# Kernel tuning notes

Hardware: AMD Instinct MI355X
Metric: run time of the kernel (lower is better)

Reference implementation:

```python
import jax, jax.numpy as jnp
import numpy as np

D = 768
H = 12
HD = D // H
NEG = -10000.0
EPS = 1e-12


def setup_inputs() -> dict:
    key = jax.random.key(0)
    ks = jax.random.split(key, 8)
    B, S = 4, 1024
    xavier = lambda k: jax.random.normal(k, (D, D), dtype=jnp.float32) * np.sqrt(2.0 / (D + D))
    return {
        "embeddings": jax.random.normal(ks[0], (B, S, D), dtype=jnp.float32),
        "padding_mask": jnp.ones((B, S), dtype=jnp.float32),
        "wq_w": xavier(ks[1]), "wq_b": jnp.zeros((D,), jnp.float32),
        "wk_w": xavier(ks[2]), "wk_b": jnp.zeros((D,), jnp.float32),
        "wv_w": xavier(ks[3]), "wv_b": jnp.zeros((D,), jnp.float32),
        "wo_w": xavier(ks[4]), "wo_b": jnp.zeros((D,), jnp.float32),
        "ln_g": jnp.ones((D,), jnp.float32), "ln_b": jnp.zeros((D,), jnp.float32),
    }


def reference(embeddings, padding_mask, wq_w, wq_b, wk_w, wk_b, wv_w, wv_b, wo_w, wo_b, ln_g, ln_b):
    B, S, _ = embeddings.shape
    # QKV projections (torch Linear: x @ W^T + b), split heads -> [B,H,S,HD]
    split = lambda t: t.reshape(B, S, H, HD).transpose(0, 2, 1, 3)
    q = split(embeddings @ wq_w.T + wq_b)
    k = split(embeddings @ wk_w.T + wk_b)
    v = split(embeddings @ wv_w.T + wv_b)
    # NOTE: original scales by sqrt(embedding_dim), not sqrt(per-head dim)
    attn = jnp.einsum("bhqd,bhkd->bhqk", q, k) / jnp.sqrt(jnp.float32(D))
    # additive padding mask, then causal masked_fill (set, not add)
    attn = attn + ((1.0 - padding_mask)[:, None, None, :] * NEG)
    causal = jnp.tril(jnp.ones((S, S), dtype=jnp.float32))
    attn = jnp.where(causal[None, None] == 0, NEG, attn)
    attn_probs = jax.nn.softmax(attn, axis=-1)  # dropout is identity at inference
    ctx = jnp.einsum("bhqk,bhkd->bhqd", attn_probs, v)
    ctx = ctx.transpose(0, 2, 1, 3).reshape(B, S, D)
    attn_out = ctx @ wo_w.T + wo_b  # keep_prob = 1.0 -> no rescale
    # residual + LayerNorm(eps=1e-12)
    x = attn_out + embeddings
    mu = jnp.mean(x, axis=-1, keepdims=True)
    var = jnp.mean((x - mu) ** 2, axis=-1, keepdims=True)
    normed = (x - mu) * jax.lax.rsqrt(var + EPS) * ln_g + ln_b
    return (normed, attn_probs)
```

## Files before the change

kernel.cpp:

```cpp
#include <hip/hip_runtime.h>
#include <hip/hip_bf16.h>

typedef __bf16 bf16x8 __attribute__((ext_vector_type(8)));
typedef float  f32x4  __attribute__((ext_vector_type(4)));

#define NEGC (-10000.0f)

static __device__ __forceinline__ void glds16(const __bf16* src, __bf16* dst) {
    __builtin_amdgcn_global_load_lds((const __attribute__((address_space(1))) unsigned int*)src,
                                     (__attribute__((address_space(3))) unsigned int*)dst, 16, 0, 0);
}

__global__ __launch_bounds__(256) void cvt_all(
    const float* __restrict__ emb, const float* __restrict__ wq, const float* __restrict__ wk,
    const float* __restrict__ wv, const float* __restrict__ wo,
    __bf16* __restrict__ Xb, __bf16* __restrict__ Wall)
{
    int blk = blockIdx.x;
    const float* src; __bf16* dst; int i;
    if (blk < 1536) {
        src = emb; dst = Xb; i = blk * 256 + threadIdx.x;
    } else {
        int b2 = blk - 1536;
        int which = b2 / 288;
        src = which == 0 ? wq : which == 1 ? wk : which == 2 ? wv : wo;
        dst = Wall + (size_t)which * 589824;
        i = (b2 - which * 288) * 256 + threadIdx.x;
    }
    f32x4 a = *(const f32x4*)(src + (size_t)i * 8);
    f32x4 b = *(const f32x4*)(src + (size_t)i * 8 + 4);
    bf16x8 o;
    o[0] = (__bf16)a[0]; o[1] = (__bf16)a[1]; o[2] = (__bf16)a[2]; o[3] = (__bf16)a[3];
    o[4] = (__bf16)b[0]; o[5] = (__bf16)b[1]; o[6] = (__bf16)b[2]; o[7] = (__bf16)b[3];
    *(bf16x8*)(dst + (size_t)i * 8) = o;
}

template<int MODE>
__global__ __launch_bounds__(256) void gemm128(
    const __bf16* __restrict__ A, const __bf16* __restrict__ Bw,
    const float* __restrict__ b0, const float* __restrict__ b1, const float* __restrict__ b2,
    __bf16* __restrict__ O0, __bf16* __restrict__ O1, __bf16* __restrict__ O2,
    const float* __restrict__ res, float* __restrict__ Yout)
{
    __shared__ __align__(16) __bf16 As[128 * 32];
    __shared__ __align__(16) __bf16 Bs[128 * 32];
    const int K = 768;
    int tid = threadIdx.x;
    int l = tid & 63, w = tid >> 6;
    int lo = l & 15, hi = l >> 4;
    int m0 = blockIdx.x * 128, n0 = blockIdx.y * 128;
    int wr = w >> 1, wc = w & 1;

    f32x4 acc[4][4] = {};

    int srow = w * 16 + (l >> 2);
    int scol = (l & 3) * 8;
    const __bf16* gA = A + (size_t)(m0 + srow) * K + scol;
    const __bf16* gB = Bw + (size_t)(n0 + srow) * K + scol;
    __bf16* lA = As + w * 512 + l * 8;
    __bf16* lB = Bs + w * 512 + l * 8;

    for (int k0 = 0; k0 < K; k0 += 32) {
        if (k0) __syncthreads();
        glds16(gA + k0, lA);
        glds16(gA + (size_t)64 * K + k0, lA + 2048);
        glds16(gB + k0, lB);
        glds16(gB + (size_t)64 * K + k0, lB + 2048);
        __syncthreads();

        bf16x8 af[4], bfr[4];
#pragma unroll
        for (int mi = 0; mi < 4; mi++)
            af[mi] = *(const bf16x8*)(As + (wr * 64 + mi * 16 + lo) * 32 + hi * 8);
#pragma unroll
        for (int ni = 0; ni < 4; ni++)
            bfr[ni] = *(const bf16x8*)(Bs + (wc * 64 + ni * 16 + lo) * 32 + hi * 8);
#pragma unroll
        for (int mi = 0; mi < 4; mi++)
#pragma unroll
            for (int ni = 0; ni < 4; ni++)
                acc[mi][ni] = __builtin_amdgcn_mfma_f32_16x16x32_bf16(af[mi], bfr[ni], acc[mi][ni], 0, 0, 0);
    }

    if constexpr (MODE == 0) {
        int which = n0 / 768;
        const float* bias = which == 0 ? b0 : (which == 1 ? b1 : b2);
        __bf16* O = which == 0 ? O0 : (which == 1 ? O1 : O2);
        int nbase = n0 - which * 768;
#pragma unroll
        for (int mi = 0; mi < 4; mi++)
#pragma unroll
            for (int ni = 0; ni < 4; ni++) {
                int within = nbase + wc * 64 + ni * 16 + lo;
                float bv = bias[within];
                int h = within >> 6, d = within & 63;
#pragma unroll
                for (int i = 0; i < 4; i++) {
                    int m = m0 + wr * 64 + mi * 16 + hi * 4 + i;
                    int bb = m >> 10, s = m & 1023;
                    O[(size_t)((bb * 12 + h) * 1024 + s) * 64 + d] = (__bf16)(acc[mi][ni][i] + bv);
                }
            }
    } else {
#pragma unroll
        for (int mi = 0; mi < 4; mi++)
#pragma unroll
            for (int ni = 0; ni < 4; ni++) {
                int n = n0 + wc * 64 + ni * 16 + lo;
                float bv = b0[n];
#pragma unroll
                for (int i = 0; i < 4; i++) {
                    int m = m0 + wr * 64 + mi * 16 + hi * 4 + i;
                    size_t idx = (size_t)m * 768 + n;
                    Yout[idx] = acc[mi][ni][i] + bv + res[idx];
                }
            }
    }
}

__global__ __launch_bounds__(256) void attn_kernel(
    const __bf16* __restrict__ Q, const __bf16* __restrict__ K, const __bf16* __restrict__ V,
    const float* __restrict__ pmask, float* __restrict__ Pout, __bf16* __restrict__ ctx)
{
    int wgid = blockIdx.x;
    int xcd = wgid & 7;
    int t = wgid >> 3;
    int bh = xcd * 6 + (t % 6);
    int y = t / 6;
    int b = bh / 12, h = bh - b * 12;
    int q0 = y * 64;
    int tid = threadIdx.x, l = tid & 63, w = tid >> 6;
    int lo = l & 15, hi = l >> 4;
    int qw = q0 + w * 16;

    const __bf16* Qh = Q + (size_t)bh * 65536;
    const __bf16* Kh = K + (size_t)bh * 65536;
    const __bf16* Vh = V + (size_t)bh * 65536;
    float* Ph = Pout + (size_t)bh * 1048576;
    const float* pm = pmask + b * 1024;

    __shared__ __align__(16) __bf16 Ks[2][64][64];
    __shared__ __align__(16) __bf16 vt[2][64][72];
    __shared__ __align__(16) __bf16 plds[4][16][72];

    const float scale = 0.036084391824351615f;

    bf16x8 qf0 = *(const bf16x8*)(Qh + (size_t)(qw + lo) * 64 + hi * 8);
    bf16x8 qf1 = *(const bf16x8*)(Qh + (size_t)(qw + lo) * 64 + 32 + hi * 8);

    int srow = tid >> 3;
    int scb  = (tid & 7) ^ (srow & 7);
    __bf16* ldst0 = &Ks[0][0][0] + tid * 8;

#define STAGE_K(buf, kt)  do {                                             \
        glds16(Kh + (size_t)((kt) * 64 + srow) * 64 + scb * 8,             \
               ldst0 + (buf) * 4096);                                      \
        glds16(Kh + (size_t)((kt) * 64 + 32 + srow) * 64 + scb * 8,        \
               ldst0 + (buf) * 4096 + 2048);                               \
    } while (0)

#define KFRAG(buf, kn, dh) \
    (*(const bf16x8*)(&Ks[buf][(kn) * 16 + lo][(((dh) * 4 + hi) ^ (lo & 7)) * 8]))

    float lsum[4] = {};
    STAGE_K(0, 0);
    __syncthreads();
    for (int kt = 0; kt <= y; kt++) {
        int cur = kt & 1;
        if (kt < y) STAGE_K(cur ^ 1, kt + 1);
        int k0 = kt * 64;
        float pad[4];
#pragma unroll
        for (int kn = 0; kn < 4; kn++) pad[kn] = (1.0f - pm[k0 + kn * 16 + lo]) * NEGC;
        f32x4 s[4] = {};
        __builtin_amdgcn_s_setprio(1);
#pragma unroll
        for (int kn = 0; kn < 4; kn++) {
            s[kn] = __builtin_amdgcn_mfma_f32_16x16x32_bf16(qf0, KFRAG(cur, kn, 0), s[kn], 0, 0, 0);
            s[kn] = __builtin_amdgcn_mfma_f32_16x16x32_bf16(qf1, KFRAG(cur, kn, 1), s[kn], 0, 0, 0);
        }
        __builtin_amdgcn_s_setprio(0);
#pragma unroll
        for (int kn = 0; kn < 4; kn++) {
            int c = k0 + kn * 16 + lo;
#pragma unroll
            for (int i = 0; i < 4; i++) {
                int r = qw + hi * 4 + i;
                float a = s[kn][i] * scale + pad[kn];
                if (c > r) a = NEGC;
                lsum[i] += __expf(a);
            }
        }
        __syncthreads();
    }

    float invl[4];
#pragma unroll
    for (int i = 0; i < 4; i++) {
        float s = lsum[i];
        s += __shfl_xor(s, 1);
        s += __shfl_xor(s, 2);
        s += __shfl_xor(s, 4);
        s += __shfl_xor(s, 8);
        invl[i] = 1.0f / s;
    }

    int vrow = tid >> 2, vcol = (tid & 3) * 16;
    bf16x8 va, vb;
    {
        STAGE_K(0, 0);
        const __bf16* vp = Vh + (size_t)vrow * 64 + vcol;
        va = *(const bf16x8*)vp; vb = *(const bf16x8*)(vp + 8);
#pragma unroll
        for (int j = 0; j < 8; j++) vt[0][vcol + j][vrow] = va[j];
#pragma unroll
        for (int j = 0; j < 8; j++) vt[0][vcol + 8 + j][vrow] = vb[j];
        if (y > 0) {
            const __bf16* vp1 = Vh + (size_t)(64 + vrow) * 64 + vcol;
            va = *(const bf16x8*)vp1; vb = *(const bf16x8*)(vp1 + 8);
        }
        __syncthreads();
    }

    f32x4 cacc[4] = {};
    for (int kt = 0; kt <= y; kt++) {
        int cur = kt & 1;
        if (kt < y) STAGE_K(cur ^ 1, kt + 1);
        int k0 = kt * 64;
        float pad[4];
#pragma unroll
        for (int kn = 0; kn < 4; kn++) pad[kn] = (1.0f - pm[k0 + kn * 16 + lo]) * NEGC;
        f32x4 s[4] = {};
        __builtin_amdgcn_s_setprio(1);
#pragma unroll
        for (int kn = 0; kn < 4; kn++) {
            s[kn] = __builtin_amdgcn_mfma_f32_16x16x32_bf16(qf0, KFRAG(cur, kn, 0), s[kn], 0, 0, 0);
            s[kn] = __builtin_amdgcn_mfma_f32_16x16x32_bf16(qf1, KFRAG(cur, kn, 1), s[kn], 0, 0, 0);
        }
        __builtin_amdgcn_s_setprio(0);
#pragma unroll
        for (int kn = 0; kn < 4; kn++) {
            int c = k0 + kn * 16 + lo;
#pragma unroll
            for (int i = 0; i < 4; i++) {
                int r = qw + hi * 4 + i;
                float a = s[kn][i] * scale + pad[kn];
                if (c > r) a = NEGC;
                float p = __expf(a) * invl[i];
                Ph[(size_t)r * 1024 + c] = p;
                plds[w][hi * 4 + i][kn * 16 + lo] = (__bf16)p;
            }
        }
        __builtin_amdgcn_s_setprio(1);
#pragma unroll
        for (int ks = 0; ks < 2; ks++) {
            bf16x8 pf = *(const bf16x8*)(&plds[w][lo][ks * 32 + hi * 8]);
#pragma unroll
            for (int dt = 0; dt < 4; dt++) {
                bf16x8 vf = *(const bf16x8*)(&vt[cur][dt * 16 + lo][ks * 32 + hi * 8]);
                cacc[dt] = __builtin_amdgcn_mfma_f32_16x16x32_bf16(pf, vf, cacc[dt], 0, 0, 0);
            }
        }
        __builtin_amdgcn_s_setprio(0);
        if (kt < y) {
#pragma unroll
            for (int j = 0; j < 8; j++) vt[cur ^ 1][vcol + j][vrow] = va[j];
#pragma unroll
            for (int j = 0; j < 8; j++) vt[cur ^ 1][vcol + 8 + j][vrow] = vb[j];
            if (kt + 1 < y) {
                const __bf16* vp = Vh + (size_t)((kt + 2) * 64 + vrow) * 64 + vcol;
                va = *(const bf16x8*)vp; vb = *(const bf16x8*)(vp + 8);
            }
        }
        __syncthreads();
    }

#pragma unroll
    for (int dt = 0; dt < 4; dt++) {
#pragma unroll
        for (int i = 0; i < 4; i++) {
            int m = b * 1024 + qw + hi * 4 + i;
            int n = h * 64 + dt * 16 + lo;
            ctx[(size_t)m * 768 + n] = (__bf16)cacc[dt][i];
        }
    }

    for (int c = (y + 1) * 64 + lo * 4; c < 1024; c += 64) {
#pragma unroll
        for (int i = 0; i < 4; i++) {
            f32x4 z = {};
            *(f32x4*)(Ph + (size_t)(qw + hi * 4 + i) * 1024 + c) = z;
        }
    }
#undef STAGE_K
#undef KFRAG
}

__global__ __launch_bounds__(256) void ln_kernel(
    const float* __restrict__ Y, const float* __restrict__ g, const float* __restrict__ bta,
    float* __restrict__ out)
{
    int row = blockIdx.x * 4 + (threadIdx.x >> 6);
    int l = threadIdx.x & 63;
    const float* yr = Y + (size_t)row * 768;
    f32x4 v0 = *(const f32x4*)(yr + l * 4);
    f32x4 v1 = *(const f32x4*)(yr + 256 + l * 4);
    f32x4 v2 = *(const f32x4*)(yr + 512 + l * 4);
    float s = v0[0] + v0[1] + v0[2] + v0[3] + v1[0] + v1[1] + v1[2] + v1[3]
            + v2[0] + v2[1] + v2[2] + v2[3];
#pragma unroll
    for (int m = 1; m < 64; m <<= 1) s += __shfl_xor(s, m);
    float mu = s * (1.0f / 768.0f);
    float ss = 0.0f;
#pragma unroll
    for (int j = 0; j < 4; j++) {
        float d0 = v0[j] - mu, d1 = v1[j] - mu, d2 = v2[j] - mu;
        ss += d0 * d0 + d1 * d1 + d2 * d2;
    }
#pragma unroll
    for (int m = 1; m < 64; m <<= 1) ss += __shfl_xor(ss, m);
    float r = rsqrtf(ss * (1.0f / 768.0f) + 1e-12f);
    float* orow = out + (size_t)row * 768;
#pragma unroll
    for (int c = 0; c < 3; c++) {
        f32x4 v = (c == 0) ? v0 : ((c == 1) ? v1 : v2);
        int col = c * 256 + l * 4;
        f32x4 gg = *(const f32x4*)(g + col);
        f32x4 bb = *(const f32x4*)(bta + col);
        f32x4 o;
#pragma unroll
        for (int j = 0; j < 4; j++) o[j] = (v[j] - mu) * r * gg[j] + bb[j];
        *(f32x4*)(orow + col) = o;
    }
}

extern "C" void kernel_launch(void* const* d_in, const int* in_sizes, int n_in,
                              void* d_out, int out_size, void* d_ws, size_t ws_size,
                              hipStream_t stream)
{
    const float* emb   = (const float*)d_in[0];
    const float* pmask = (const float*)d_in[1];
    const float* wq = (const float*)d_in[2];  const float* bq = (const float*)d_in[3];
    const float* wk = (const float*)d_in[4];  const float* bk = (const float*)d_in[5];
    const float* wv = (const float*)d_in[6];  const float* bv = (const float*)d_in[7];
    const float* wo = (const float*)d_in[8];  const float* bo = (const float*)d_in[9];
    const float* lng = (const float*)d_in[10]; const float* lnb = (const float*)d_in[11];

    __bf16* Xb   = (__bf16*)d_ws;
    __bf16* Wall = Xb + 4096 * 768;
    __bf16* Qb   = Wall + 4 * 589824;
    __bf16* Kb   = Qb + 3145728;
    __bf16* Vb   = Kb + 3145728;
    __bf16* Cb   = Vb + 3145728;
    float*  Yf   = (float*)(Cb + 3145728);

    float* normed = (float*)d_out;
    float* probs  = normed + (size_t)4096 * 768;

    cvt_all<<<2688, 256, 0, stream>>>(emb, wq, wk, wv, wo, Xb, Wall);

    gemm128<0><<<dim3(32, 18), 256, 0, stream>>>(Xb, Wall, bq, bk, bv, Qb, Kb, Vb, nullptr, nullptr);
    attn_kernel<<<768, 256, 0, stream>>>(Qb, Kb, Vb, pmask, probs, Cb);
    gemm128<1><<<dim3(32, 6), 256, 0, stream>>>(Cb, Wall + 3 * 589824, bo, nullptr, nullptr,
                                                nullptr, nullptr, nullptr, emb, Yf);
    ln_kernel<<<1024, 256, 0, stream>>>(Yf, lng, lnb, normed);
}
```

Before: 124.7 us.

## Use exp2 with folded log2e and software-pipeline V loads and P stores

Folds log2(e) into the score scale and the mask constants so softmax uses exp2f instead of __expf. The second attention pass is unrolled by two with double-buffered V register loads issued two tiles ahead. Each tile's probability stores to global memory are deferred to the next iteration so they overlap the next QK MFMA work. This is meant to hide global load and store latency behind compute, at the cost of extra registers holding the deferred probabilities and the second V buffer.

After: 132.8 us. 6.5% more time.

```diff
diff --git a/kernel.cpp b/kernel.cpp
--- a/kernel.cpp
+++ b/kernel.cpp
@@ -4,7 +4,8 @@
 typedef __bf16 bf16x8 __attribute__((ext_vector_type(8)));
 typedef float  f32x4  __attribute__((ext_vector_type(4)));
 
-#define NEGC (-10000.0f)
+#define NEGC  (-10000.0f)
+#define NEGL2 (-14426.950408889634f)
 
 static __device__ __forceinline__ void glds16(const __bf16* src, __bf16* dst) {
     __builtin_amdgcn_global_load_lds((const __attribute__((address_space(1))) unsigned int*)src,
@@ -143,7 +144,7 @@
     __shared__ __align__(16) __bf16 vt[2][64][72];
     __shared__ __align__(16) __bf16 plds[4][16][72];
 
-    const float scale = 0.036084391824351615f;
+    const float scl2 = 0.036084391824351615f * 1.4426950408889634f;
 
     bf16x8 qf0 = *(const bf16x8*)(Qh + (size_t)(qw + lo) * 64 + hi * 8);
     bf16x8 qf1 = *(const bf16x8*)(Qh + (size_t)(qw + lo) * 64 + 32 + hi * 8);
@@ -171,7 +172,7 @@
         int k0 = kt * 64;
         float pad[4];
 #pragma unroll
-        for (int kn = 0; kn < 4; kn++) pad[kn] = (1.0f - pm[k0 + kn * 16 + lo]) * NEGC;
+        for (int kn = 0; kn < 4; kn++) pad[kn] = (1.0f - pm[k0 + kn * 16 + lo]) * NEGL2;
         f32x4 s[4] = {};
         __builtin_amdgcn_s_setprio(1);
 #pragma unroll
@@ -186,9 +187,9 @@
 #pragma unroll
             for (int i = 0; i < 4; i++) {
                 int r = qw + hi * 4 + i;
-                float a = s[kn][i] * scale + pad[kn];
-                if (c > r) a = NEGC;
-                lsum[i] += __expf(a);
+                float a = s[kn][i] * scl2 + pad[kn];
+                if (c > r) a = NEGL2;
+                lsum[i] += exp2f(a);
             }
         }
         __syncthreads();
@@ -206,74 +207,102 @@
     }
 
     int vrow = tid >> 2, vcol = (tid & 3) * 16;
-    bf16x8 va, vb;
+    bf16x8 va0, vb0, va1, vb1;
+    float pv[4][4];
+    int pk0 = 0;
+
     {
         STAGE_K(0, 0);
         const __bf16* vp = Vh + (size_t)vrow * 64 + vcol;
-        va = *(const bf16x8*)vp; vb = *(const bf16x8*)(vp + 8);
-#pragma unroll
-        for (int j = 0; j < 8; j++) vt[0][vcol + j][vrow] = va[j];
-#pragma unroll
-        for (int j = 0; j < 8; j++) vt[0][vcol + 8 + j][vrow] = vb[j];
+        va0 = *(const bf16x8*)vp; vb0 = *(const bf16x8*)(vp + 8);
         if (y > 0) {
             const __bf16* vp1 = Vh + (size_t)(64 + vrow) * 64 + vcol;
-            va = *(const bf16x8*)vp1; vb = *(const bf16x8*)(vp1 + 8);
-        }
+            va1 = *(const bf16x8*)vp1; vb1 = *(const bf16x8*)(vp1 + 8);
+        }
+#pragma unroll
+        for (int j = 0; j < 8; j++) vt[0][vcol + j][vrow] = va0[j];
+#pragma unroll
+        for (int j = 0; j < 8; j++) vt[0][vcol + 8 + j][vrow] = vb0[j];
         __syncthreads();
     }
 
     f32x4 cacc[4] = {};
-    for (int kt = 0; kt <= y; kt++) {
-        int cur = kt & 1;
-        if (kt < y) STAGE_K(cur ^ 1, kt + 1);
-        int k0 = kt * 64;
-        float pad[4];
-#pragma unroll
-        for (int kn = 0; kn < 4; kn++) pad[kn] = (1.0f - pm[k0 + kn * 16 + lo]) * NEGC;
-        f32x4 s[4] = {};
-        __builtin_amdgcn_s_setprio(1);
-#pragma unroll
-        for (int kn = 0; kn < 4; kn++) {
-            s[kn] = __builtin_amdgcn_mfma_f32_16x16x32_bf16(qf0, KFRAG(cur, kn, 0), s[kn], 0, 0, 0);
-            s[kn] = __builtin_amdgcn_mfma_f32_16x16x32_bf16(qf1, KFRAG(cur, kn, 1), s[kn], 0, 0, 0);
-        }
-        __builtin_amdgcn_s_setprio(0);
-#pragma unroll
-        for (int kn = 0; kn < 4; kn++) {
-            int c = k0 + kn * 16 + lo;
-#pragma unroll
-            for (int i = 0; i < 4; i++) {
-                int r = qw + hi * 4 + i;
-                float a = s[kn][i] * scale + pad[kn];
-                if (c > r) a = NEGC;
-                float p = __expf(a) * invl[i];
-                Ph[(size_t)r * 1024 + c] = p;
-                plds[w][hi * 4 + i][kn * 16 + lo] = (__bf16)p;
-            }
-        }
-        __builtin_amdgcn_s_setprio(1);
-#pragma unroll
-        for (int ks = 0; ks < 2; ks++) {
-            bf16x8 pf = *(const bf16x8*)(&plds[w][lo][ks * 32 + hi * 8]);
-#pragma unroll
-            for (int dt = 0; dt < 4; dt++) {
-                bf16x8 vf = *(const bf16x8*)(&vt[cur][dt * 16 + lo][ks * 32 + hi * 8]);
-                cacc[dt] = __builtin_amdgcn_mfma_f32_16x16x32_bf16(pf, vf, cacc[dt], 0, 0, 0);
-            }
-        }
-        __builtin_amdgcn_s_setprio(0);
-        if (kt < y) {
-#pragma unroll
-            for (int j = 0; j < 8; j++) vt[cur ^ 1][vcol + j][vrow] = va[j];
-#pragma unroll
-            for (int j = 0; j < 8; j++) vt[cur ^ 1][vcol + 8 + j][vrow] = vb[j];
-            if (kt + 1 < y) {
-                const __bf16* vp = Vh + (size_t)((kt + 2) * 64 + vrow) * 64 + vcol;
-                va = *(const bf16x8*)vp; vb = *(const bf16x8*)(vp + 8);
-            }
-        }
-        __syncthreads();
-    }
+
+#define PASS2_BODY(ktv, lva, lvb, sva, svb) do {                               \
+        int cur_ = (ktv) & 1;                                                  \
+        if ((ktv) < y) STAGE_K(cur_ ^ 1, (ktv) + 1);                           \
+        if ((ktv) + 2 <= y) {                                                  \
+            const __bf16* vp_ = Vh + (size_t)(((ktv) + 2) * 64 + vrow) * 64 + vcol; \
+            lva = *(const bf16x8*)vp_; lvb = *(const bf16x8*)(vp_ + 8);        \
+        }                                                                      \
+        int k0_ = (ktv) * 64;                                                  \
+        float pad_[4];                                                         \
+        _Pragma("unroll")                                                      \
+        for (int kn = 0; kn < 4; kn++)                                         \
+            pad_[kn] = (1.0f - pm[k0_ + kn * 16 + lo]) * NEGL2;                \
+        if ((ktv) > 0) {             \
+            _Pragma("unroll")                                                  \
+            for (int kn = 0; kn < 4; kn++) {                                   \
+                int c_ = pk0 + kn * 16 + lo;                                   \
+                _Pragma("unroll")                                              \
+                for (int i = 0; i < 4; i++)                                    \
+                    Ph[(size_t)(qw + hi * 4 + i) * 1024 + c_] = pv[kn][i];     \
+            }                                                                  \
+        }                                                                      \
+        f32x4 s_[4] = {};                                                      \
+        __builtin_amdgcn_s_setprio(1);                                         \
+        _Pragma("unroll")                                                      \
+        for (int kn = 0; kn < 4; kn++) {                                       \
+            s_[kn] = __builtin_amdgcn_mfma_f32_16x16x32_bf16(qf0, KFRAG(cur_, kn, 0), s_[kn], 0, 0, 0); \
+            s_[kn] = __builtin_amdgcn_mfma_f32_16x16x32_bf16(qf1, KFRAG(cur_, kn, 1), s_[kn], 0, 0, 0); \
+        }                                                                      \
+        __builtin_amdgcn_s_setprio(0);                                         \
+        _Pragma("unroll")                                                      \
+        for (int kn = 0; kn < 4; kn++) {                                       \
+            int c_ = k0_ + kn * 16 + lo;                                       \
+            _Pragma("unroll")                                                  \
+            for (int i = 0; i < 4; i++) {                                      \
+                int r_ = qw + hi * 4 + i;                                      \
+                float a_ = s_[kn][i] * scl2 + pad_[kn];                        \
+                if (c_ > r_) a_ = NEGL2;                                       \
+                float p_ = exp2f(a_) * invl[i];       \
+                pv[kn][i] = p_;                                                \
+                plds[w][hi * 4 + i][kn * 16 + lo] = (__bf16)p_;                \
+            }                                                                  \
+        }                                                                      \
+        pk0 = k0_;                                                             \
+        __builtin_amdgcn_s_setprio(1);                                         \
+        _Pragma("unroll")                                                      \
+        for (int ks = 0; ks < 2; ks++) {                                       \
+            bf16x8 pf_ = *(const bf16x8*)(&plds[w][lo][ks * 32 + hi * 8]);     \
+            _Pragma("unroll")                                                  \
+            for (int dt = 0; dt < 4; dt++) {                                   \
+                bf16x8 vf_ = *(const bf16x8*)(&vt[cur_][dt * 16 + lo][ks * 32 + hi * 8]); \
+                cacc[dt] = __builtin_amdgcn_mfma_f32_16x16x32_bf16(pf_, vf_, cacc[dt], 0, 0, 0); \
+            }                                                                  \
+        }                                                                      \
+        __builtin_amdgcn_s_setprio(0);                                         \
+        if ((ktv) + 1 <= y) {                                                  \
+            _Pragma("unroll")                                                  \
+            for (int j = 0; j < 8; j++) vt[((ktv) + 1) & 1][vcol + j][vrow] = sva[j];     \
+            _Pragma("unroll")                                                  \
+            for (int j = 0; j < 8; j++) vt[((ktv) + 1) & 1][vcol + 8 + j][vrow] = svb[j]; \
+        }                                                                      \
+        __syncthreads();                                                       \
+    } while (0)
+
+    for (int kt = 0; kt <= y; kt += 2) {
+        PASS2_BODY(kt, va0, vb0, va1, vb1);
+        if (kt + 1 <= y) PASS2_BODY(kt + 1, va1, vb1, va0, vb0);
+    }
+#pragma unroll
+    for (int kn = 0; kn < 4; kn++) {
+        int c = pk0 + kn * 16 + lo;
+#pragma unroll
+        for (int i = 0; i < 4; i++)
+            Ph[(size_t)(qw + hi * 4 + i) * 1024 + c] = pv[kn][i];
+    }
+#undef PASS2_BODY
 
 #pragma unroll
     for (int dt = 0; dt < 4; dt++) {
```
